# Kernel tuning notes

Hardware: AMD Instinct MI355X
Metric: run time of the kernel (lower is better)

## Reference

```python
import jax, jax.numpy as jnp
import numpy as np

LN_EPS = 1e-5
DEN_EPS = 1e-5


def _layernorm(x, gamma, beta):
    mu = jnp.mean(x, axis=-1, keepdims=True)
    var = jnp.mean((x - mu) ** 2, axis=-1, keepdims=True)
    return (x - mu) * jax.lax.rsqrt(var + LN_EPS) * gamma + beta


def setup_inputs() -> dict:
    key = jax.random.key(0)
    ks = jax.random.split(key, 10)
    B, T, Fin, D = 4, 1024, 256, 128
    s = 0.02
    return {
        "x": jax.random.normal(ks[0], (B, T, Fin), jnp.float32),
        "S0": jnp.zeros((B, 1, D, D), jnp.float32),
        "Z0": jnp.zeros((B, 1, D), jnp.float32),
        "ln_gamma": jnp.ones((Fin,), jnp.float32),
        "ln_beta": jnp.zeros((Fin,), jnp.float32),
        "Wk": jax.random.normal(ks[1], (D, Fin), jnp.float32) * s,
        "Wq": jax.random.normal(ks[2], (D, Fin), jnp.float32) * s,
        "Wv": jax.random.normal(ks[3], (D, Fin), jnp.float32) * s,
        "W1": jax.random.normal(ks[4], (D, D), jnp.float32) * s,
        "b1": jnp.zeros((D,), jnp.float32),
        "W2": jax.random.normal(ks[5], (D, D), jnp.float32) * s,
        "b2": jnp.zeros((D,), jnp.float32),
        "Ws": jax.random.normal(ks[6], (D, Fin), jnp.float32) * s,
        "bs": jnp.zeros((D,), jnp.float32),
    }


def reference(x, S0, Z0, ln_gamma, ln_beta, Wk, Wq, Wv, W1, b1, W2, b2, Ws, bs):
    xn = _layernorm(x, ln_gamma, ln_beta)            # [B,T,Fin]
    phi = lambda z: jax.nn.elu(z) + 1.0
    K = phi(jnp.einsum('btf,df->btd', xn, Wk))       # [B,T,D]
    Q = phi(jnp.einsum('btf,df->btd', xn, Wq))
    V = jnp.einsum('btf,df->btd', xn, Wv)
    # running-sum aggregation of K outer V, seeded by carried state
    KV = jnp.einsum('bti,btj->btij', K, V)           # [B,T,D,D]
    S = jnp.cumsum(KV, axis=1) + S0                  # [B,T,D,D]
    Z = jnp.cumsum(K, axis=1) + Z0                   # [B,T,D]
    num = jnp.einsum('bti,btil->btl', Q, S)          # [B,T,D]
    den = jnp.einsum('btl,btl->bt', Q, Z)[..., None] + DEN_EPS
    out = num / den
    out = jax.nn.relu(jnp.einsum('btd,ed->bte', out, W1) + b1)
    out = jax.nn.relu(jnp.einsum('btd,ed->bte', out, W2) + b2)
    out = out + jnp.einsum('btf,df->btd', xn, Ws) + bs
    return (out, S, Z)
```

## Files before the change

### kernel.cpp

```cpp
#include <hip/hip_runtime.h>
#include <math.h>

#define BB 4
#define TT 1024
#define FIN 256
#define DD 128
#define CL 16
#define NC 64
#define ROWS (BB*TT)

__global__ __launch_bounds__(256) void k_ln_qkv(
    const float* __restrict__ x, const float* __restrict__ gamma, const float* __restrict__ beta,
    const float* __restrict__ Wk, const float* __restrict__ Wq, const float* __restrict__ Wv,
    const float* __restrict__ Ws, const float* __restrict__ bs,
    float* __restrict__ Kp, float* __restrict__ Qp, float* __restrict__ Vp, float* __restrict__ XSp)
{
    __shared__ float xt[8][FIN];
    const int tid  = threadIdx.x;
    const int row0 = blockIdx.x * 8;

    {
        const int r = tid >> 5, l = tid & 31;
        const float* xr = x + (size_t)(row0 + r) * FIN + l * 8;
        float v[8];
        #pragma unroll
        for (int k = 0; k < 8; ++k) v[k] = xr[k];
        float s = 0.f, sq = 0.f;
        #pragma unroll
        for (int k = 0; k < 8; ++k) { s += v[k]; sq += v[k] * v[k]; }
        #pragma unroll
        for (int m = 16; m >= 1; m >>= 1) {
            s  += __shfl_xor(s,  m, 64);
            sq += __shfl_xor(sq, m, 64);
        }
        const float mu  = s * (1.0f / FIN);
        const float var = sq * (1.0f / FIN) - mu * mu;
        const float rs  = rsqrtf(var + 1e-5f);
        #pragma unroll
        for (int k = 0; k < 8; ++k) {
            const int f = l * 8 + k;
            xt[r][f] = (v[k] - mu) * rs * gamma[f] + beta[f];
        }
    }
    __syncthreads();

    const int m0 = tid >> 7;
    const int d  = tid & 127;
    const int m1 = (tid + 256) >> 7;
    const float* W0 = (m0 == 0 ? Wk : Wq) + (size_t)d * FIN;
    const float* W1r = (m1 == 2 ? Wv : Ws) + (size_t)d * FIN;

    float acc0[8], acc1[8];
    #pragma unroll
    for (int r = 0; r < 8; ++r) { acc0[r] = 0.f; acc1[r] = 0.f; }

    for (int k4 = 0; k4 < FIN / 4; ++k4) {
        const float4 w0 = ((const float4*)W0)[k4];
        const float4 w1 = ((const float4*)W1r)[k4];
        #pragma unroll
        for (int r = 0; r < 8; ++r) {
            const float4 xv = ((const float4*)xt[r])[k4];
            acc0[r] += w0.x * xv.x + w0.y * xv.y + w0.z * xv.z + w0.w * xv.w;
            acc1[r] += w1.x * xv.x + w1.y * xv.y + w1.z * xv.z + w1.w * xv.w;
        }
    }

    float* dst0 = (m0 == 0 ? Kp : Qp);
    float* dst1 = (m1 == 2 ? Vp : XSp);
    const float bsv = (m1 == 3) ? bs[d] : 0.f;
    #pragma unroll
    for (int r = 0; r < 8; ++r) {
        float a = acc0[r];
        a = (a > 0.f) ? (a + 1.f) : expf(a);
        dst0[(size_t)(row0 + r) * DD + d] = a;
        dst1[(size_t)(row0 + r) * DD + d] = acc1[r] + bsv;
    }
}

__global__ __launch_bounds__(256) void k_chunksum(
    const float* __restrict__ Kp, const float* __restrict__ Vp,
    float* __restrict__ SKV, float* __restrict__ SK)
{
    __shared__ float Kb[CL][DD];
    __shared__ float Vb[CL][DD];
    const int tid = threadIdx.x;
    const int c = blockIdx.x & (NC - 1);
    const int b = blockIdx.x >> 6;
    const size_t base = (size_t)(b * TT + c * CL) * DD;

    #pragma unroll
    for (int q = 0; q < 2; ++q) {
        const int fi = q * 256 + tid;
        ((float4*)&Kb[0][0])[fi] = ((const float4*)(Kp + base))[fi];
        ((float4*)&Vb[0][0])[fi] = ((const float4*)(Vp + base))[fi];
    }
    __syncthreads();

    const int j = tid & 127, hi = tid >> 7;
    float acc[64];
    #pragma unroll
    for (int w = 0; w < 64; ++w) acc[w] = 0.f;

    for (int t = 0; t < CL; ++t) {
        const float vj = Vb[t][j];
        #pragma unroll
        for (int w4 = 0; w4 < 16; ++w4) {
            const float4 kf = *(const float4*)&Kb[t][hi * 64 + w4 * 4];
            acc[w4 * 4 + 0] += kf.x * vj;
            acc[w4 * 4 + 1] += kf.y * vj;
            acc[w4 * 4 + 2] += kf.z * vj;
            acc[w4 * 4 + 3] += kf.w * vj;
        }
    }

    float* out = SKV + (size_t)(b * NC + c) * DD * DD;
    #pragma unroll
    for (int w = 0; w < 64; ++w) {
        const int i = hi * 64 + w;
        out[(size_t)i * DD + j] = acc[w];
    }
    if (tid < DD) {
        float s = 0.f;
        #pragma unroll
        for (int t = 0; t < CL; ++t) s += Kb[t][tid];
        SK[(size_t)(b * NC + c) * DD + tid] = s;
    }
}

__global__ __launch_bounds__(256) void k_prefix(
    const float* __restrict__ SKV, const float* __restrict__ SK,
    const float* __restrict__ S0, const float* __restrict__ Z0,
    float* __restrict__ Sout, float* __restrict__ Zout)
{
    const int gid = blockIdx.x * 256 + threadIdx.x;
    const int b = gid >> 14, e = gid & 16383;
    float acc = S0[(size_t)b * 16384 + e];
    const float* p = SKV + (size_t)b * NC * 16384 + e;
    float* so = Sout + (size_t)b * TT * 16384 + (size_t)(CL - 1) * 16384 + e;
    for (int c0 = 0; c0 < NC; c0 += 8) {
        float v[8];
        #pragma unroll
        for (int q = 0; q < 8; ++q) v[q] = p[(size_t)(c0 + q) * 16384];
        #pragma unroll
        for (int q = 0; q < 8; ++q) { acc += v[q]; so[(size_t)(c0 + q) * CL * 16384] = acc; }
    }
    if (gid < BB * DD) {
        const int b2 = gid >> 7, i = gid & 127;
        float z = Z0[b2 * DD + i];
        const float* pk = SK + (size_t)b2 * NC * DD + i;
        float* zo = Zout + ((size_t)b2 * TT + CL - 1) * DD + i;
        for (int c0 = 0; c0 < NC; c0 += 8) {
            float v[8];
            #pragma unroll
            for (int q = 0; q < 8; ++q) v[q] = pk[(size_t)(c0 + q) * DD];
            #pragma unroll
            for (int q = 0; q < 8; ++q) { z += v[q]; zo[(size_t)(c0 + q) * CL * DD] = z; }
        }
    }
}

__global__ __launch_bounds__(256) void k_num_mlp(
    const float* __restrict__ Qp, const float* __restrict__ Kp, const float* __restrict__ Vp,
    const float* __restrict__ XSp, const float* __restrict__ S0, const float* __restrict__ Z0,
    const float* __restrict__ W1, const float* __restrict__ b1,
    const float* __restrict__ W2, const float* __restrict__ b2,
    const float* Sce,
    float* Zout,
    float* __restrict__ Oout)
{
    __shared__ float Qb[CL][132];
    __shared__ float Kb[CL][132];
    __shared__ float Vb[CL][DD];
    __shared__ float Ab[CL][CL];
    __shared__ float zs[DD];
    __shared__ float red[2][CL][DD];
    __shared__ float h0[CL][DD];
    __shared__ float h1[CL][DD];
    __shared__ float parr[CL][256];
    __shared__ float denl[CL];

    const int tid = threadIdx.x;
    const int c = blockIdx.x & (NC - 1);
    const int b = blockIdx.x >> 6;
    const size_t rbase = (size_t)(b * TT + c * CL);
    const int d = tid & 127, s = tid >> 7;

    float4 w1r[16], w2r[16];
    #pragma unroll
    for (int k4 = 0; k4 < 16; ++k4) {
        w1r[k4] = *(const float4*)(W1 + (size_t)d * DD + s * 64 + k4 * 4);
        w2r[k4] = *(const float4*)(W2 + (size_t)d * DD + s * 64 + k4 * 4);
    }

    #pragma unroll
    for (int q = 0; q < 2; ++q) {
        const int idx = q * 256 + tid;
        const int t = idx >> 5, jq = idx & 31;
        *(float4*)&Qb[t][jq * 4] = *(const float4*)(Qp + (rbase + t) * DD + jq * 4);
        *(float4*)&Kb[t][jq * 4] = *(const float4*)(Kp + (rbase + t) * DD + jq * 4);
        ((float4*)&Vb[0][0])[idx] = ((const float4*)(Vp + rbase * DD))[idx];
    }
    if (tid < DD)
        zs[tid] = (c == 0) ? Z0[b * DD + tid] : Zout[(rbase - 1) * DD + tid];
    __syncthreads();

    {
        const int t = tid >> 4, u = tid & 15;
        float a = 0.f;
        #pragma unroll
        for (int k4 = 0; k4 < 32; ++k4) {
            const float4 q4 = *(const float4*)&Qb[t][k4 * 4];
            const float4 kv = *(const float4*)&Kb[u][k4 * 4];
            a += q4.x * kv.x + q4.y * kv.y + q4.z * kv.z + q4.w * kv.w;
        }
        const float am = (u <= t) ? a : 0.f;
        Ab[t][u] = am;
        float dz = 0.f;
        #pragma unroll
        for (int kk = 0; kk < 8; ++kk) dz += Qb[t][u * 8 + kk] * zs[u * 8 + kk];
        float r = am + dz;
        #pragma unroll
        for (int m = 1; m <= 8; m <<= 1) r += __shfl_xor(r, m, 64);
        if (u == 0) denl[t] = r + 1e-5f;
    }

    if (tid < DD) {
        float z = zs[tid];
        for (int t = 0; t < CL - 1; ++t) {
            z += Kb[t][tid];
            Zout[(rbase + t) * DD + tid] = z;
        }
    }
    __syncthreads();

    {
        float nt[CL];
        #pragma unroll
        for (int t = 0; t < CL; ++t) nt[t] = 0.f;
        const float* sst = (c == 0) ? (S0 + (size_t)b * 16384)
                                    : (Sce + (rbase - 1) * 16384);
        #pragma unroll 4
        for (int k4 = s * 16; k4 < s * 16 + 16; ++k4) {
            const int k = k4 * 4;
            const float sv0 = sst[(size_t)(k + 0) * DD + d];
            const float sv1 = sst[(size_t)(k + 1) * DD + d];
            const float sv2 = sst[(size_t)(k + 2) * DD + d];
            const float sv3 = sst[(size_t)(k + 3) * DD + d];
            #pragma unroll
            for (int t = 0; t < CL; ++t) {
                const float4 q4 = *(const float4*)&Qb[t][k];
                nt[t] += q4.x * sv0 + q4.y * sv1 + q4.z * sv2 + q4.w * sv3;
            }
        }
        #pragma unroll
        for (int t = 0; t < CL; ++t) red[s][t][d] = nt[t];
    }
    __syncthreads();

    #pragma unroll
    for (int tl = 0; tl < 8; ++tl) {
        const int t = s * 8 + tl;
        float num = red[0][t][d] + red[1][t][d];
        #pragma unroll
        for (int u = 0; u < CL; ++u) num += Ab[t][u] * Vb[u][d];
        h0[t][d] = num / denl[t];
    }
    __syncthreads();

    #pragma unroll
    for (int r = 0; r < 16; ++r) {
        float pp = 0.f;
        #pragma unroll
        for (int k4 = 0; k4 < 16; ++k4) {
            const float4 xv = *(const float4*)&h0[r][s * 64 + k4 * 4];
            pp += w1r[k4].x * xv.x + w1r[k4].y * xv.y + w1r[k4].z * xv.z + w1r[k4].w * xv.w;
        }
        parr[r][tid] = pp;
    }
    __syncthreads();
    #pragma unroll
    for (int q = 0; q < 8; ++q) {
        const int f = q * 256 + tid;
        const int r = f >> 7, dd2 = f & 127;
        h1[r][dd2] = fmaxf(parr[r][dd2] + parr[r][dd2 + 128] + b1[dd2], 0.f);
    }
    __syncthreads();

    #pragma unroll
    for (int r = 0; r < 16; ++r) {
        float pp = 0.f;
        #pragma unroll
        for (int k4 = 0; k4 < 16; ++k4) {
            const float4 xv = *(const float4*)&h1[r][s * 64 + k4 * 4];
            pp += w2r[k4].x * xv.x + w2r[k4].y * xv.y + w2r[k4].z * xv.z + w2r[k4].w * xv.w;
        }
        parr[r][tid] = pp;
    }
    __syncthreads();
    #pragma unroll
    for (int q = 0; q < 8; ++q) {
        const int f = q * 256 + tid;
        const int r = f >> 7, dd2 = f & 127;
        const float hv = fmaxf(parr[r][dd2] + parr[r][dd2 + 128] + b2[dd2], 0.f);
        Oout[rbase * DD + f] = hv + XSp[rbase * DD + f];
    }
}

__global__ __launch_bounds__(256) void k_scan(
    const float* __restrict__ Kp, const float* __restrict__ Vp,
    const float* __restrict__ S0, float* Sout)
{
    __shared__ float Kb[CL][64];
    __shared__ float Vb[CL][DD];
    const int tid = threadIdx.x;
    const int ih  = blockIdx.x & 1;
    const int c   = (blockIdx.x >> 1) & (NC - 1);
    const int b   = blockIdx.x >> 7;
    const int i0  = ih * 64;
    const size_t rbase = (size_t)(b * TT + c * CL);

    {
        const float4* Vsrc = (const float4*)(Vp + rbase * DD);
        ((float4*)&Vb[0][0])[tid]       = Vsrc[tid];
        ((float4*)&Vb[0][0])[256 + tid] = Vsrc[256 + tid];
        const int tv = tid >> 4, gk = tid & 15;
        *(float4*)&Kb[tv][gk * 4] = *(const float4*)(Kp + (rbase + tv) * DD + i0 + gk * 4);
    }

    const int g = tid & 31, h = tid >> 5;
    float4 acc[8];
    {
        const float* src = (c == 0) ? (S0 + (size_t)b * 16384)
                                    : (Sout + ((size_t)(b * TT) + c * CL - 1) * 16384);
        #pragma unroll
        for (int w = 0; w < 8; ++w)
            acc[w] = *(const float4*)(src + (size_t)(i0 + w * 8 + h) * DD + g * 4);
    }
    __syncthreads();

    float* sbase = Sout + rbase * 16384 + (size_t)i0 * DD + g * 4;
    for (int t = 0; t < CL - 1; ++t) {
        const float4 v4 = *(const float4*)&Vb[t][g * 4];
        #pragma unroll
        for (int w = 0; w < 8; ++w) {
            const float kk = Kb[t][w * 8 + h];
            acc[w].x += kk * v4.x; acc[w].y += kk * v4.y;
            acc[w].z += kk * v4.z; acc[w].w += kk * v4.w;
            *(float4*)(sbase + (size_t)t * 16384 + (size_t)(w * 8 + h) * DD) = acc[w];
        }
    }
}

extern "C" void kernel_launch(void* const* d_in, const int* in_sizes, int n_in,
                              void* d_out, int out_size, void* d_ws, size_t ws_size,
                              hipStream_t stream)
{
    const float* x  = (const float*)d_in[0];
    const float* S0 = (const float*)d_in[1];
    const float* Z0 = (const float*)d_in[2];
    const float* g  = (const float*)d_in[3];
    const float* be = (const float*)d_in[4];
    const float* Wk = (const float*)d_in[5];
    const float* Wq = (const float*)d_in[6];
    const float* Wv = (const float*)d_in[7];
    const float* W1 = (const float*)d_in[8];
    const float* b1 = (const float*)d_in[9];
    const float* W2 = (const float*)d_in[10];
    const float* b2 = (const float*)d_in[11];
    const float* Ws = (const float*)d_in[12];
    const float* bs = (const float*)d_in[13];

    float* outp = (float*)d_out;
    float* Sout = outp + (size_t)ROWS * DD;
    float* Zout = Sout + (size_t)BB * TT * DD * DD;

    float* ws  = (float*)d_ws;
    float* Kp  = ws;
    float* Qp  = Kp + (size_t)ROWS * DD;
    float* Vp  = Qp + (size_t)ROWS * DD;
    float* XSp = Vp + (size_t)ROWS * DD;
    float* SKV = XSp + (size_t)ROWS * DD;
    float* SK  = SKV + (size_t)BB * NC * DD * DD;

    k_ln_qkv  <<<ROWS / 8, 256, 0, stream>>>(x, g, be, Wk, Wq, Wv, Ws, bs, Kp, Qp, Vp, XSp);
    k_chunksum<<<BB * NC, 256, 0, stream>>>(Kp, Vp, SKV, SK);
    k_prefix  <<<BB * DD * DD / 256, 256, 0, stream>>>(SKV, SK, S0, Z0, Sout, Zout);
    k_num_mlp <<<BB * NC, 256, 0, stream>>>(Qp, Kp, Vp, XSp, S0, Z0,
                                            W1, b1, W2, b2, Sout, Zout, outp);
    k_scan    <<<BB * NC * 2, 256, 0, stream>>>(Kp, Vp, S0, Sout);
}
```

Measured before the change: 391.0 us.

## Fuse chunk-sum into LN/QKV kernel, split scan finer, use nontemporal stores

Merges the layernorm/QKV projection kernel with the chunk K-outer-V summation, so each block now handles one 16-row chunk and builds the chunk sums from K and V held in shared memory instead of reloading them from global memory. This drops one launch and a K/V round trip, but cuts the first kernel's grid from 512 to 256 blocks and doubles its per-thread accumulators. The scan kernel is split into four row-quarters per chunk instead of two, for more parallelism. Its large S output is written with nontemporal stores to reduce cache pollution.

```diff
diff --git a/kernel.cpp b/kernel.cpp
--- a/kernel.cpp
+++ b/kernel.cpp
@@ -9,27 +9,39 @@
 #define NC 64
 #define ROWS (BB*TT)
 
-__global__ __launch_bounds__(256) void k_ln_qkv(
+typedef float f32x4_t __attribute__((ext_vector_type(4)));
+
+static __device__ __forceinline__ void nt_store4(float* p, float4 v) {
+    f32x4_t t; t.x = v.x; t.y = v.y; t.z = v.z; t.w = v.w;
+    __builtin_nontemporal_store(t, (f32x4_t*)p);
+}
+
+__global__ __launch_bounds__(256) void k_ln_qkv_cs(
     const float* __restrict__ x, const float* __restrict__ gamma, const float* __restrict__ beta,
     const float* __restrict__ Wk, const float* __restrict__ Wq, const float* __restrict__ Wv,
     const float* __restrict__ Ws, const float* __restrict__ bs,
-    float* __restrict__ Kp, float* __restrict__ Qp, float* __restrict__ Vp, float* __restrict__ XSp)
-{
-    __shared__ float xt[8][FIN];
+    float* __restrict__ Kp, float* __restrict__ Qp, float* __restrict__ Vp, float* __restrict__ XSp,
+    float* __restrict__ SKV, float* __restrict__ SK)
+{
+    __shared__ float xt[CL][FIN];
+    __shared__ float Kb[CL][DD];
+    __shared__ float Vb[CL][DD];
     const int tid  = threadIdx.x;
-    const int row0 = blockIdx.x * 8;
-
-    {
-        const int r = tid >> 5, l = tid & 31;
-        const float* xr = x + (size_t)(row0 + r) * FIN + l * 8;
-        float v[8];
-        #pragma unroll
-        for (int k = 0; k < 8; ++k) v[k] = xr[k];
+    const int c    = blockIdx.x & (NC - 1);
+    const int b    = blockIdx.x >> 6;
+    const int row0 = (b * TT + c * CL);
+
+    {
+        const int r = tid >> 4, l = tid & 15;
+        const float* xr = x + (size_t)(row0 + r) * FIN + l * 16;
+        float v[16];
+        #pragma unroll
+        for (int k = 0; k < 16; ++k) v[k] = xr[k];
         float s = 0.f, sq = 0.f;
         #pragma unroll
-        for (int k = 0; k < 8; ++k) { s += v[k]; sq += v[k] * v[k]; }
-        #pragma unroll
-        for (int m = 16; m >= 1; m >>= 1) {
+        for (int k = 0; k < 16; ++k) { s += v[k]; sq += v[k] * v[k]; }
+        #pragma unroll
+        for (int m = 8; m >= 1; m >>= 1) {
             s  += __shfl_xor(s,  m, 64);
             sq += __shfl_xor(sq, m, 64);
         }
@@ -37,8 +49,8 @@
         const float var = sq * (1.0f / FIN) - mu * mu;
         const float rs  = rsqrtf(var + 1e-5f);
         #pragma unroll
-        for (int k = 0; k < 8; ++k) {
-            const int f = l * 8 + k;
+        for (int k = 0; k < 16; ++k) {
+            const int f = l * 16 + k;
             xt[r][f] = (v[k] - mu) * rs * gamma[f] + beta[f];
         }
     }
@@ -47,18 +59,18 @@
     const int m0 = tid >> 7;
     const int d  = tid & 127;
     const int m1 = (tid + 256) >> 7;
-    const float* W0 = (m0 == 0 ? Wk : Wq) + (size_t)d * FIN;
+    const float* W0  = (m0 == 0 ? Wk : Wq) + (size_t)d * FIN;
     const float* W1r = (m1 == 2 ? Wv : Ws) + (size_t)d * FIN;
 
-    float acc0[8], acc1[8];
-    #pragma unroll
-    for (int r = 0; r < 8; ++r) { acc0[r] = 0.f; acc1[r] = 0.f; }
+    float acc0[CL], acc1[CL];
+    #pragma unroll
+    for (int r = 0; r < CL; ++r) { acc0[r] = 0.f; acc1[r] = 0.f; }
 
     for (int k4 = 0; k4 < FIN / 4; ++k4) {
         const float4 w0 = ((const float4*)W0)[k4];
         const float4 w1 = ((const float4*)W1r)[k4];
         #pragma unroll
-        for (int r = 0; r < 8; ++r) {
+        for (int r = 0; r < CL; ++r) {
             const float4 xv = ((const float4*)xt[r])[k4];
             acc0[r] += w0.x * xv.x + w0.y * xv.y + w0.z * xv.z + w0.w * xv.w;
             acc1[r] += w1.x * xv.x + w1.y * xv.y + w1.z * xv.z + w1.w * xv.w;
@@ -69,61 +81,50 @@
     float* dst1 = (m1 == 2 ? Vp : XSp);
     const float bsv = (m1 == 3) ? bs[d] : 0.f;
     #pragma unroll
-    for (int r = 0; r < 8; ++r) {
+    for (int r = 0; r < CL; ++r) {
         float a = acc0[r];
         a = (a > 0.f) ? (a + 1.f) : expf(a);
+        acc0[r] = a;
         dst0[(size_t)(row0 + r) * DD + d] = a;
-        dst1[(size_t)(row0 + r) * DD + d] = acc1[r] + bsv;
-    }
-}
-
-__global__ __launch_bounds__(256) void k_chunksum(
-    const float* __restrict__ Kp, const float* __restrict__ Vp,
-    float* __restrict__ SKV, float* __restrict__ SK)
-{
-    __shared__ float Kb[CL][DD];
-    __shared__ float Vb[CL][DD];
-    const int tid = threadIdx.x;
-    const int c = blockIdx.x & (NC - 1);
-    const int b = blockIdx.x >> 6;
-    const size_t base = (size_t)(b * TT + c * CL) * DD;
-
-    #pragma unroll
-    for (int q = 0; q < 2; ++q) {
-        const int fi = q * 256 + tid;
-        ((float4*)&Kb[0][0])[fi] = ((const float4*)(Kp + base))[fi];
-        ((float4*)&Vb[0][0])[fi] = ((const float4*)(Vp + base))[fi];
-    }
-    __syncthreads();
-
-    const int j = tid & 127, hi = tid >> 7;
-    float acc[64];
-    #pragma unroll
-    for (int w = 0; w < 64; ++w) acc[w] = 0.f;
-
-    for (int t = 0; t < CL; ++t) {
-        const float vj = Vb[t][j];
-        #pragma unroll
-        for (int w4 = 0; w4 < 16; ++w4) {
-            const float4 kf = *(const float4*)&Kb[t][hi * 64 + w4 * 4];
-            acc[w4 * 4 + 0] += kf.x * vj;
-            acc[w4 * 4 + 1] += kf.y * vj;
-            acc[w4 * 4 + 2] += kf.z * vj;
-            acc[w4 * 4 + 3] += kf.w * vj;
-        }
-    }
-
-    float* out = SKV + (size_t)(b * NC + c) * DD * DD;
-    #pragma unroll
-    for (int w = 0; w < 64; ++w) {
-        const int i = hi * 64 + w;
-        out[(size_t)i * DD + j] = acc[w];
-    }
-    if (tid < DD) {
+        const float vv = acc1[r] + bsv;
+        dst1[(size_t)(row0 + r) * DD + d] = vv;
+        if (m0 == 0) {
+            Kb[r][d] = a;
+            Vb[r][d] = vv;
+        }
+    }
+
+    if (m0 == 0) {
         float s = 0.f;
         #pragma unroll
-        for (int t = 0; t < CL; ++t) s += Kb[t][tid];
-        SK[(size_t)(b * NC + c) * DD + tid] = s;
+        for (int r = 0; r < CL; ++r) s += acc0[r];
+        SK[(size_t)(b * NC + c) * DD + d] = s;
+    }
+    __syncthreads();
+
+    {
+        const int j = tid & 127, hi = tid >> 7;
+        float acc[64];
+        #pragma unroll
+        for (int w = 0; w < 64; ++w) acc[w] = 0.f;
+
+        for (int t = 0; t < CL; ++t) {
+            const float vj = Vb[t][j];
+            #pragma unroll
+            for (int w4 = 0; w4 < 16; ++w4) {
+                const float4 kf = *(const float4*)&Kb[t][hi * 64 + w4 * 4];
+                acc[w4 * 4 + 0] += kf.x * vj;
+                acc[w4 * 4 + 1] += kf.y * vj;
+                acc[w4 * 4 + 2] += kf.z * vj;
+                acc[w4 * 4 + 3] += kf.w * vj;
+            }
+        }
+        float* out = SKV + (size_t)(b * NC + c) * DD * DD;
+        #pragma unroll
+        for (int w = 0; w < 64; ++w) {
+            const int i = hi * 64 + w;
+            out[(size_t)i * DD + j] = acc[w];
+        }
     }
 }
 
@@ -310,30 +311,32 @@
     const float* __restrict__ Kp, const float* __restrict__ Vp,
     const float* __restrict__ S0, float* Sout)
 {
-    __shared__ float Kb[CL][64];
+    __shared__ float Kb[CL][32];
     __shared__ float Vb[CL][DD];
     const int tid = threadIdx.x;
-    const int ih  = blockIdx.x & 1;
-    const int c   = (blockIdx.x >> 1) & (NC - 1);
-    const int b   = blockIdx.x >> 7;
-    const int i0  = ih * 64;
+    const int ih  = blockIdx.x & 3;
+    const int c   = (blockIdx.x >> 2) & (NC - 1);
+    const int b   = blockIdx.x >> 8;
+    const int i0  = ih * 32;
     const size_t rbase = (size_t)(b * TT + c * CL);
 
     {
         const float4* Vsrc = (const float4*)(Vp + rbase * DD);
         ((float4*)&Vb[0][0])[tid]       = Vsrc[tid];
         ((float4*)&Vb[0][0])[256 + tid] = Vsrc[256 + tid];
-        const int tv = tid >> 4, gk = tid & 15;
-        *(float4*)&Kb[tv][gk * 4] = *(const float4*)(Kp + (rbase + tv) * DD + i0 + gk * 4);
+        if (tid < 128) {
+            const int tv = tid >> 3, gk = tid & 7;
+            *(float4*)&Kb[tv][gk * 4] = *(const float4*)(Kp + (rbase + tv) * DD + i0 + gk * 4);
+        }
     }
 
     const int g = tid & 31, h = tid >> 5;
-    float4 acc[8];
+    float4 acc[4];
     {
         const float* src = (c == 0) ? (S0 + (size_t)b * 16384)
                                     : (Sout + ((size_t)(b * TT) + c * CL - 1) * 16384);
         #pragma unroll
-        for (int w = 0; w < 8; ++w)
+        for (int w = 0; w < 4; ++w)
             acc[w] = *(const float4*)(src + (size_t)(i0 + w * 8 + h) * DD + g * 4);
     }
     __syncthreads();
@@ -342,11 +345,11 @@
     for (int t = 0; t < CL - 1; ++t) {
         const float4 v4 = *(const float4*)&Vb[t][g * 4];
         #pragma unroll
-        for (int w = 0; w < 8; ++w) {
+        for (int w = 0; w < 4; ++w) {
             const float kk = Kb[t][w * 8 + h];
             acc[w].x += kk * v4.x; acc[w].y += kk * v4.y;
             acc[w].z += kk * v4.z; acc[w].w += kk * v4.w;
-            *(float4*)(sbase + (size_t)t * 16384 + (size_t)(w * 8 + h) * DD) = acc[w];
+            nt_store4(sbase + (size_t)t * 16384 + (size_t)(w * 8 + h) * DD, acc[w]);
         }
     }
 }
@@ -382,10 +385,10 @@
     float* SKV = XSp + (size_t)ROWS * DD;
     float* SK  = SKV + (size_t)BB * NC * DD * DD;
 
-    k_ln_qkv  <<<ROWS / 8, 256, 0, stream>>>(x, g, be, Wk, Wq, Wv, Ws, bs, Kp, Qp, Vp, XSp);
-    k_chunksum<<<BB * NC, 256, 0, stream>>>(Kp, Vp, SKV, SK);
-    k_prefix  <<<BB * DD * DD / 256, 256, 0, stream>>>(SKV, SK, S0, Z0, Sout, Zout);
-    k_num_mlp <<<BB * NC, 256, 0, stream>>>(Qp, Kp, Vp, XSp, S0, Z0,
-                                            W1, b1, W2, b2, Sout, Zout, outp);
-    k_scan    <<<BB * NC * 2, 256, 0, stream>>>(Kp, Vp, S0, Sout);
-}
+    k_ln_qkv_cs<<<BB * NC, 256, 0, stream>>>(x, g, be, Wk, Wq, Wv, Ws, bs,
+                                             Kp, Qp, Vp, XSp, SKV, SK);
+    k_prefix   <<<BB * DD * DD / 256, 256, 0, stream>>>(SKV, SK, S0, Z0, Sout, Zout);
+    k_num_mlp  <<<BB * NC, 256, 0, stream>>>(Qp, Kp, Vp, XSp, S0, Z0,
+                                             W1, b1, W2, b2, Sout, Zout, outp);
+    k_scan     <<<BB * NC * 4, 256, 0, stream>>>(Kp, Vp, S0, Sout);
+}
```

After: 384.7 us. No clear change (-1.6%).
